# Kernel optimization log

Hardware: AMD Instinct MI355X
Metric: run time of the kernel (lower is better)

Reference implementation:

```python
import jax, jax.numpy as jnp
import numpy as np

EPS_COS = 1e-8   # torch F.cosine_similarity eps
EPS_L1 = 1e-12   # torch F.normalize eps


def setup_inputs() -> dict:
    key = jax.random.key(0)
    k1, k2, k3, k4 = jax.random.split(key, 4)
    B, D, C = 32768, 768, 200
    features = jax.random.normal(k1, (B, D), dtype=jnp.float32)
    centers = jax.random.normal(k2, (C, D), dtype=jnp.float32)
    labels = jax.random.randint(k3, (B,), 0, C)
    labelled_or_not = jax.random.randint(k4, (B,), 0, 2).astype(jnp.bool_)
    return {"features": features, "centers": centers, "labels": labels,
            "labelled_or_not": labelled_or_not}


def reference(features, centers, labels, labelled_or_not):
    # cosine similarity: x.y / (max(|x|,eps) * max(|y|,eps))
    fn = features / jnp.maximum(jnp.linalg.norm(features, axis=1, keepdims=True), EPS_COS)
    cn = centers / jnp.maximum(jnp.linalg.norm(centers, axis=1, keepdims=True), EPS_COS)
    cos = jnp.einsum('bd,cd->bc', fn, cn)  # [B, C]

    # per-sample sign logic: label column -> +|cos|, all others -> -|cos|
    a = jnp.abs(cos)
    is_label = jax.nn.one_hot(labels, cos.shape[1], dtype=jnp.bool_)  # [B, C]
    signed = jnp.where(is_label, a, -a)

    # L1 normalize per row (||row||_1 == sum of |cos| regardless of signs)
    l1 = jnp.sum(a, axis=1, keepdims=True)
    normed = signed / jnp.maximum(l1, EPS_L1)

    # only labelled rows contribute (row-wise normalize is independent per row,
    # so masking after is equivalent to boolean-indexing before)
    contrib = jnp.where(labelled_or_not[:, None], normed, 0.0)
    return -jnp.sum(contrib)
```

## Files before the change

### kernel.cpp

```cpp
#include <hip/hip_runtime.h>
#include <hip/hip_bf16.h>

#define NROWS 32768
#define DIMS  768
#define NC    200
#define CPAD  256
#define KSTEP 32
#define NSTEP (DIMS / KSTEP)
#define ROWSB 64

typedef __attribute__((ext_vector_type(8))) short short8;
typedef __attribute__((ext_vector_type(4))) float f32x4;

#define WAITV4 asm volatile("s_waitcnt vmcnt(4)" ::: "memory")
#define WAITV2 asm volatile("s_waitcnt vmcnt(2)" ::: "memory")
#define WAITL0 asm volatile("s_waitcnt lgkmcnt(0)" ::: "memory")
#define BAR    __builtin_amdgcn_s_barrier()

__device__ __forceinline__ unsigned pk_bf16(float lo, float hi) {
  union { __hip_bfloat162 h; unsigned u; } c;
  c.h = __float22bfloat162_rn(make_float2(lo, hi));
  return c.u;
}

__global__ __launch_bounds__(256) void prep_centers_k(const float* __restrict__ centers,
                                                      short* __restrict__ cnb2,
                                                      float* __restrict__ out) {
  const int c = blockIdx.x;
  const int tid = threadIdx.x;
  if (c == 0 && tid == 0) out[0] = 0.f;
  if (c >= NC) {
    for (int d = tid; d < DIMS; d += 256)
      cnb2[(d >> 5) * (CPAD * KSTEP) + c * KSTEP + (d & 31)] = 0;
    return;
  }
  float ssq = 0.f;
  for (int d = tid; d < DIMS; d += 256) {
    float v = centers[c * DIMS + d];
    ssq += v * v;
  }
#pragma unroll
  for (int off = 32; off > 0; off >>= 1) ssq += __shfl_down(ssq, off);
  __shared__ float red[4];
  const int wid = tid >> 6, lane = tid & 63;
  if (lane == 0) red[wid] = ssq;
  __syncthreads();
  const float tot = red[0] + red[1] + red[2] + red[3];
  const float inv = 1.f / fmaxf(sqrtf(tot), 1e-8f);
  for (int d = tid; d < DIMS; d += 256) {
    const float v = centers[c * DIMS + d] * inv;
    union { __hip_bfloat16 h; short s; } cv;
    cv.h = __float2bfloat16(v);
    cnb2[(d >> 5) * (CPAD * KSTEP) + c * KSTEP + (d & 31)] = cv.s;
  }
}

__global__ __launch_bounds__(512, 4) void cos_loss_k(
    const float* __restrict__ feats,
    const short* __restrict__ cnb2,
    const int* __restrict__ labels,
    const int* __restrict__ labelled,
    float* __restrict__ out) {
  const int tid = threadIdx.x;
  const int wid = tid >> 6;
  const int lane = tid & 63;
  const int rowBase = blockIdx.x * ROWSB;

  __shared__ short As[2][ROWSB][32];
  __shared__ float invs[ROWSB];
  __shared__ int   labLds[ROWSB];
  __shared__ int   lblLds[ROWSB];
  __shared__ float l1part[4][ROWSB];
  __shared__ float alpart[4][ROWSB];

  if (tid < ROWSB) {
    labLds[tid] = labels[rowBase + tid];
    lblLds[tid] = labelled[rowBase + tid];
  }

  if (wid < 4) {
    const int m = lane & 15;
    const int kg = lane >> 4;
    const int rdq = (kg ^ ((m >> 1) & 3)) * 8;
    const short* bp = cnb2 + (size_t)(wid * 64 + m) * KSTEP + kg * 8;

    f32x4 acc[4][4];
#pragma unroll
    for (int mi = 0; mi < 4; ++mi)
#pragma unroll
      for (int ni = 0; ni < 4; ++ni) acc[mi][ni] = (f32x4){0.f, 0.f, 0.f, 0.f};

    short8 B0[4], B1[4];

#define LOADB(B, s) do {                                                 \
    const short* bs_ = bp + (size_t)(s) * (CPAD * KSTEP);                \
    B[0] = *(const short8*)(bs_ + 0 * (16 * KSTEP));                     \
    B[1] = *(const short8*)(bs_ + 1 * (16 * KSTEP));                     \
    B[2] = *(const short8*)(bs_ + 2 * (16 * KSTEP));                     \
    B[3] = *(const short8*)(bs_ + 3 * (16 * KSTEP));                     \
  } while (0)

#define CCOMPUTE(ab, B) do {                                             \
    short8 af[4];                                                        \
    _Pragma("unroll")                                                    \
    for (int mi = 0; mi < 4; ++mi)                                       \
      af[mi] = *(const short8*)(&As[(ab)][mi * 16 + m][rdq]);            \
    _Pragma("unroll")                                                    \
    for (int mi = 0; mi < 4; ++mi)                                       \
      _Pragma("unroll")                                                  \
      for (int ni = 0; ni < 4; ++ni)                                     \
        acc[mi][ni] = __builtin_amdgcn_mfma_f32_16x16x32_bf16(           \
            af[mi], B[ni], acc[mi][ni], 0, 0, 0);                        \
  } while (0)

    LOADB(B0, 0);
    LOADB(B1, 1);
    WAITV4;
    BAR;

    for (int s = 0; s < NSTEP; s += 2) {
      CCOMPUTE(0, B0);
      { const int s2 = (s + 2 < NSTEP) ? s + 2 : NSTEP - 1; LOADB(B0, s2); }
      WAITV4;
      BAR;
      CCOMPUTE(1, B1);
      { const int s3 = (s + 3 < NSTEP) ? s + 3 : NSTEP - 1; LOADB(B1, s3); }
      WAITV4;
      BAR;
    }
#undef LOADB
#undef CCOMPUTE

    BAR;

#pragma unroll
    for (int mi = 0; mi < 4; ++mi) {
      float l1r[4] = {0.f, 0.f, 0.f, 0.f};
      float alr[4] = {0.f, 0.f, 0.f, 0.f};
      float iv[4];
      int labr[4];
#pragma unroll
      for (int r = 0; r < 4; ++r) {
        const int row = mi * 16 + kg * 4 + r;
        iv[r] = invs[row];
        labr[r] = labLds[row];
      }
#pragma unroll
      for (int ni = 0; ni < 4; ++ni) {
        const int col = wid * 64 + ni * 16 + m;
#pragma unroll
        for (int r = 0; r < 4; ++r) {
          const float a = fabsf(acc[mi][ni][r] * iv[r]);
          l1r[r] += a;
          if (col == labr[r]) alr[r] += a;
        }
      }
#pragma unroll
      for (int r = 0; r < 4; ++r) {
#pragma unroll
        for (int off = 1; off < 16; off <<= 1) {
          l1r[r] += __shfl_xor(l1r[r], off);
          alr[r] += __shfl_xor(alr[r], off);
        }
      }
      if (m == 0) {
#pragma unroll
        for (int r = 0; r < 4; ++r) {
          l1part[wid][mi * 16 + kg * 4 + r] = l1r[r];
          alpart[wid][mi * 16 + kg * 4 + r] = alr[r];
        }
      }
    }
  } else {
    const int pt = (wid - 4) * 64 + lane;
    const int arow = pt >> 2;
    const int aq   = pt & 3;
    const int aswz = (arow >> 1) & 3;
    const float* asrc = feats + (size_t)(rowBase + arow) * DIMS + aq * 8;
    short* adst0 = &As[0][arow][(aq ^ aswz) * 8];
    short* adst1 = &As[1][arow][(aq ^ aswz) * 8];

    float ssq = 0.f;
    float4 S0lo, S0hi, S1lo, S1hi;

#define LOADA(P, s) do {                                                 \
    const float* ap_ = asrc + (s) * KSTEP;                               \
    P##lo = *(const float4*)(ap_);                                       \
    P##hi = *(const float4*)(ap_ + 4);                                   \
  } while (0)

#define WRITEA(P, dst, guard) do {                                       \
    if (guard) {                                                         \
      ssq += P##lo.x*P##lo.x + P##lo.y*P##lo.y                           \
           + P##lo.z*P##lo.z + P##lo.w*P##lo.w;                          \
      ssq += P##hi.x*P##hi.x + P##hi.y*P##hi.y                           \
           + P##hi.z*P##hi.z + P##hi.w*P##hi.w;                          \
    }                                                                    \
    union { short8 s8; unsigned u[4]; } p_;                              \
    p_.u[0] = pk_bf16(P##lo.x, P##lo.y);                                 \
    p_.u[1] = pk_bf16(P##lo.z, P##lo.w);                                 \
    p_.u[2] = pk_bf16(P##hi.x, P##hi.y);                                 \
    p_.u[3] = pk_bf16(P##hi.z, P##hi.w);                                 \
    *(short8*)(dst) = p_.s8;                                             \
  } while (0)

    LOADA(S0, 0);
    LOADA(S1, 1);
    WAITV2;
    WRITEA(S0, adst0, true);
    WAITL0;
    BAR;

    for (int s = 0; s < NSTEP; s += 2) {
      { const int s2 = (s + 2 < NSTEP) ? s + 2 : NSTEP - 1; LOADA(S0, s2); }
      WAITV2;
      WRITEA(S1, adst1, (s + 1 < NSTEP));
      WAITL0;
      BAR;
      { const int s3 = (s + 3 < NSTEP) ? s + 3 : NSTEP - 1; LOADA(S1, s3); }
      WAITV2;
      WRITEA(S0, adst0, (s + 2 < NSTEP));
      WAITL0;
      BAR;
    }
#undef LOADA
#undef WRITEA

    ssq += __shfl_xor(ssq, 1);
    ssq += __shfl_xor(ssq, 2);
    if ((lane & 3) == 0) invs[arow] = 1.f / fmaxf(sqrtf(ssq), 1e-8f);
    WAITL0;
    BAR;
  }

  __syncthreads();

  if (tid < ROWSB) {
    const float L = l1part[0][tid] + l1part[1][tid] + l1part[2][tid] + l1part[3][tid];
    const float A = alpart[0][tid] + alpart[1][tid] + alpart[2][tid] + alpart[3][tid];
    float c = lblLds[tid] ? (L - 2.f * A) / fmaxf(L, 1e-12f) : 0.f;
#pragma unroll
    for (int off = 1; off < 64; off <<= 1) c += __shfl_xor(c, off);
    if (tid == 0) atomicAdd(out, c);
  }
}

extern "C" void kernel_launch(void* const* d_in, const int* in_sizes, int n_in,
                              void* d_out, int out_size, void* d_ws, size_t ws_size,
                              hipStream_t stream) {
  const float* feats = (const float*)d_in[0];
  const float* centers = (const float*)d_in[1];
  const int* labels = (const int*)d_in[2];
  const int* labelled = (const int*)d_in[3];
  float* out = (float*)d_out;
  short* cnb2 = (short*)d_ws;

  prep_centers_k<<<CPAD, 256, 0, stream>>>(centers, cnb2, out);
  cos_loss_k<<<NROWS / ROWSB, 512, 0, stream>>>(feats, cnb2, labels, labelled, out);
}
```

Measured before the change: 35.90 us.

## Deepen feature prefetch to three stages and interleave B loads with MFMAs

```diff
diff --git a/kernel.cpp b/kernel.cpp
--- a/kernel.cpp
+++ b/kernel.cpp
@@ -13,7 +13,6 @@
 typedef __attribute__((ext_vector_type(4))) float f32x4;
 
 #define WAITV4 asm volatile("s_waitcnt vmcnt(4)" ::: "memory")
-#define WAITV2 asm volatile("s_waitcnt vmcnt(2)" ::: "memory")
 #define WAITL0 asm volatile("s_waitcnt lgkmcnt(0)" ::: "memory")
 #define BAR    __builtin_amdgcn_s_barrier()
 
@@ -68,15 +67,8 @@
 
   __shared__ short As[2][ROWSB][32];
   __shared__ float invs[ROWSB];
-  __shared__ int   labLds[ROWSB];
-  __shared__ int   lblLds[ROWSB];
   __shared__ float l1part[4][ROWSB];
   __shared__ float alpart[4][ROWSB];
-
-  if (tid < ROWSB) {
-    labLds[tid] = labels[rowBase + tid];
-    lblLds[tid] = labelled[rowBase + tid];
-  }
 
   if (wid < 4) {
     const int m = lane & 15;
@@ -90,46 +82,39 @@
 #pragma unroll
       for (int ni = 0; ni < 4; ++ni) acc[mi][ni] = (f32x4){0.f, 0.f, 0.f, 0.f};
 
-    short8 B0[4], B1[4];
-
-#define LOADB(B, s) do {                                                 \
-    const short* bs_ = bp + (size_t)(s) * (CPAD * KSTEP);                \
-    B[0] = *(const short8*)(bs_ + 0 * (16 * KSTEP));                     \
-    B[1] = *(const short8*)(bs_ + 1 * (16 * KSTEP));                     \
-    B[2] = *(const short8*)(bs_ + 2 * (16 * KSTEP));                     \
-    B[3] = *(const short8*)(bs_ + 3 * (16 * KSTEP));                     \
-  } while (0)
-
-#define CCOMPUTE(ab, B) do {                                             \
+    short8 B[4];
+
+#define BLOAD(ni, s) \
+    B[ni] = *(const short8*)(bp + (size_t)(s) * (CPAD * KSTEP) + (ni) * (16 * KSTEP))
+
+    BLOAD(0, 0); BLOAD(1, 0); BLOAD(2, 0); BLOAD(3, 0);
+    BAR;
+
+#define PHASEC(p, ab) do {                                               \
+    const int sn_ = ((p) + 1 < NSTEP) ? (p) + 1 : NSTEP - 1;             \
     short8 af[4];                                                        \
     _Pragma("unroll")                                                    \
     for (int mi = 0; mi < 4; ++mi)                                       \
       af[mi] = *(const short8*)(&As[(ab)][mi * 16 + m][rdq]);            \
+    __builtin_amdgcn_s_setprio(1);                                       \
     _Pragma("unroll")                                                    \
-    for (int mi = 0; mi < 4; ++mi)                                       \
+    for (int ni = 0; ni < 4; ++ni) {                                     \
       _Pragma("unroll")                                                  \
-      for (int ni = 0; ni < 4; ++ni)                                     \
+      for (int mi = 0; mi < 4; ++mi)                                     \
         acc[mi][ni] = __builtin_amdgcn_mfma_f32_16x16x32_bf16(           \
             af[mi], B[ni], acc[mi][ni], 0, 0, 0);                        \
-  } while (0)
-
-    LOADB(B0, 0);
-    LOADB(B1, 1);
-    WAITV4;
-    BAR;
-
-    for (int s = 0; s < NSTEP; s += 2) {
-      CCOMPUTE(0, B0);
-      { const int s2 = (s + 2 < NSTEP) ? s + 2 : NSTEP - 1; LOADB(B0, s2); }
-      WAITV4;
-      BAR;
-      CCOMPUTE(1, B1);
-      { const int s3 = (s + 3 < NSTEP) ? s + 3 : NSTEP - 1; LOADB(B1, s3); }
-      WAITV4;
-      BAR;
+      BLOAD(ni, sn_);                                                    \
+    }                                                                    \
+    __builtin_amdgcn_s_setprio(0);                                       \
+    BAR;                                                                 \
+  } while (0)
+
+    for (int p = 0; p < NSTEP; p += 2) {
+      PHASEC(p, 0);
+      PHASEC(p + 1, 1);
     }
-#undef LOADB
-#undef CCOMPUTE
+#undef BLOAD
+#undef PHASEC
 
     BAR;
 
@@ -143,7 +128,7 @@
       for (int r = 0; r < 4; ++r) {
         const int row = mi * 16 + kg * 4 + r;
         iv[r] = invs[row];
-        labr[r] = labLds[row];
+        labr[r] = labels[rowBase + row];
       }
 #pragma unroll
       for (int ni = 0; ni < 4; ++ni) {
@@ -181,7 +166,7 @@
     short* adst1 = &As[1][arow][(aq ^ aswz) * 8];
 
     float ssq = 0.f;
-    float4 S0lo, S0hi, S1lo, S1hi;
+    float4 S0lo, S0hi, S1lo, S1hi, S2lo, S2hi;
 
 #define LOADA(P, s) do {                                                 \
     const float* ap_ = asrc + (s) * KSTEP;                               \
@@ -204,27 +189,35 @@
     *(short8*)(dst) = p_.s8;                                             \
   } while (0)
 
+#define CLMP(x) (((x) < NSTEP) ? (x) : NSTEP - 1)
+#define PHASEP(p, SL, SP, dst) do {                                      \
+    LOADA(SL, CLMP((p) + 3));                                            \
+    WAITV4;                                                              \
+    WRITEA(SP, dst, (p) + 1 < NSTEP);                                    \
+    WAITL0;                                                              \
+    BAR;                                                                 \
+  } while (0)
+
     LOADA(S0, 0);
     LOADA(S1, 1);
-    WAITV2;
+    LOADA(S2, 2);
+    WAITV4;
     WRITEA(S0, adst0, true);
     WAITL0;
     BAR;
 
-    for (int s = 0; s < NSTEP; s += 2) {
-      { const int s2 = (s + 2 < NSTEP) ? s + 2 : NSTEP - 1; LOADA(S0, s2); }
-      WAITV2;
-      WRITEA(S1, adst1, (s + 1 < NSTEP));
-      WAITL0;
-      BAR;
-      { const int s3 = (s + 3 < NSTEP) ? s + 3 : NSTEP - 1; LOADA(S1, s3); }
-      WAITV2;
-      WRITEA(S0, adst0, (s + 2 < NSTEP));
-      WAITL0;
-      BAR;
+    for (int p = 0; p < NSTEP; p += 6) {
+      PHASEP(p + 0, S0, S1, adst1);
+      PHASEP(p + 1, S1, S2, adst0);
+      PHASEP(p + 2, S2, S0, adst1);
+      PHASEP(p + 3, S0, S1, adst0);
+      PHASEP(p + 4, S1, S2, adst1);
+      PHASEP(p + 5, S2, S0, adst0);
     }
 #undef LOADA
 #undef WRITEA
+#undef PHASEP
+#undef CLMP
 
     ssq += __shfl_xor(ssq, 1);
     ssq += __shfl_xor(ssq, 2);
@@ -238,7 +231,7 @@
   if (tid < ROWSB) {
     const float L = l1part[0][tid] + l1part[1][tid] + l1part[2][tid] + l1part[3][tid];
     const float A = alpart[0][tid] + alpart[1][tid] + alpart[2][tid] + alpart[3][tid];
-    float c = lblLds[tid] ? (L - 2.f * A) / fmaxf(L, 1e-12f) : 0.f;
+    float c = labelled[rowBase + tid] ? (L - 2.f * A) / fmaxf(L, 1e-12f) : 0.f;
 #pragma unroll
     for (int off = 1; off < 64; off <<= 1) c += __shfl_xor(c, off);
     if (tid == 0) atomicAdd(out, c);
```

Result: no change. 36.14 us (+0.7%).
